# Kernel tuning notes

Hardware: AMD Instinct MI355X
Metric: run time of the kernel (lower is better)

Reference implementation:

```python
import jax, jax.numpy as jnp
import numpy as np

N, D_IN, D, K = 8192, 1024, 256, 30
SCALE = D ** (-0.5)


def setup_inputs() -> dict:
    key = jax.random.key(0)
    ks = jax.random.split(key, 10)
    p = lambda k, sh: (jax.random.normal(k, sh, dtype=jnp.float32) * 0.02)
    return {
        'x_path': jax.random.normal(ks[0], (N, D_IN), dtype=jnp.float32),
        'W_fc1': p(ks[1], (D_IN, D)), 'b_fc1': jnp.zeros((D,), jnp.float32),
        'W_fc2': p(ks[2], (D, D)),   'b_fc2': jnp.zeros((D,), jnp.float32),
        'W_head': p(ks[3], (D, D)),  'b_head': jnp.zeros((D,), jnp.float32),
        'W_tail': p(ks[4], (D, D)),  'b_tail': jnp.zeros((D,), jnp.float32),
        'W_lin1': p(ks[5], (D, D)),  'b_lin1': jnp.zeros((D,), jnp.float32),
        'W_lin2': p(ks[6], (D, D)),  'b_lin2': jnp.zeros((D,), jnp.float32),
        'W_att1': p(ks[7], (D, D // 2)), 'b_att1': jnp.zeros((D // 2,), jnp.float32),
        'W_att2': p(ks[8], (D // 2, 1)), 'b_att2': jnp.zeros((1,), jnp.float32),
    }


def reference(x_path, W_fc1, b_fc1, W_fc2, b_fc2, W_head, b_head, W_tail, b_tail,
              W_lin1, b_lin1, W_lin2, b_lin2, W_att1, b_att1, W_att2, b_att2):
    # pathology_fc (eval mode, dropout = identity): 1024 -> 256 -> 256
    h = jax.nn.relu(x_path @ W_fc1 + b_fc1)
    h = jax.nn.relu(h @ W_fc2 + b_fc2)                      # [N, D]

    e_h = h @ W_head + b_head                               # [N, D]
    e_t = h @ W_tail + b_tail                               # [N, D]

    # pairwise scores + topk neighbor selection
    attn_logit = (e_h * SCALE) @ e_t.T                      # [N, N]
    topk_w, topk_i = jax.lax.top_k(attn_logit, K)           # [N, K]
    topk_prob = jax.nn.softmax(topk_w, axis=-1)             # [N, K]

    Nb_h = e_t[topk_i]                                      # gather neighbors [N, K, D]

    # gated message construction
    eh_r = topk_prob[..., None] * Nb_h + (1.0 - topk_prob)[..., None] * e_h[:, None, :]
    gate = jnp.tanh(e_h[:, None, :] + eh_r)                 # [N, K, D]

    # torch.einsum('ijkl,ijkm->ijk', Nb_h, gate): l and m summed independently
    ka_weight = Nb_h.sum(-1) * gate.sum(-1)                 # [N, K]
    ka_prob = jax.nn.softmax(ka_weight, axis=-1)            # [N, K]
    e_Nh = jnp.einsum('nk,nkd->nd', ka_prob, Nb_h)          # [N, D]

    sum_emb = jax.nn.relu((e_h + e_Nh) @ W_lin1 + b_lin1)
    bi_emb = jax.nn.relu((e_h * e_Nh) @ W_lin2 + b_lin2)
    e = sum_emb + bi_emb                                    # [N, D]

    # GlobalAttention readout
    att = jax.nn.leaky_relu(e @ W_att1 + b_att1, 0.01) @ W_att2 + b_att2   # [N, 1]
    a = jax.nn.softmax(att, axis=0)                         # softmax over nodes
    e_g = (a * e).sum(0)                                    # [D]
    return e, e_g
```

## Files before the change

### kernel.cpp

```cpp
#include <hip/hip_runtime.h>
#include <math.h>

#define NN   8192
#define DIN  1024
#define DD   256
#define TOPK 30
#define KP   40
#define CAP  88
#define NINF -3e38f

typedef short s8v  __attribute__((ext_vector_type(8)));
typedef float f16v __attribute__((ext_vector_type(16)));

__device__ __forceinline__ float wred_sum(float v) {
  v += __shfl_down(v, 32); v += __shfl_down(v, 16); v += __shfl_down(v, 8);
  v += __shfl_down(v, 4);  v += __shfl_down(v, 2);  v += __shfl_down(v, 1);
  return v;
}
__device__ __forceinline__ float wred_max(float v) {
  v = fmaxf(v, __shfl_down(v, 32)); v = fmaxf(v, __shfl_down(v, 16));
  v = fmaxf(v, __shfl_down(v, 8));  v = fmaxf(v, __shfl_down(v, 4));
  v = fmaxf(v, __shfl_down(v, 2));  v = fmaxf(v, __shfl_down(v, 1));
  return v;
}
__device__ __forceinline__ float tanh_fast(float x) {
  return 1.f - 2.f / (__expf(2.f * x) + 1.f);
}
__device__ __forceinline__ unsigned short f2bf(float x) {
  union { float f; unsigned int u; } v; v.f = x;
  unsigned int r = v.u + 0x7FFF + ((v.u >> 16) & 1);
  return (unsigned short)(r >> 16);
}
__device__ __forceinline__ bool pair_gt(float v, int i, float pv, int pi) {
  return (v > pv) || (v == pv && i < pi);
}
__device__ __forceinline__ unsigned key_pack(float f, int col) {
  unsigned b = __float_as_uint(f);
  unsigned u = ((int)b < 0) ? ~b : (b | 0x80000000u);
  return (u & 0xFFFFE000u) | (unsigned)col;
}

template<int ACT, int AOP, int ACCUM>
__global__ __launch_bounds__(128, 4)
void gemm_k(const float* __restrict__ A, const float* __restrict__ A2,
            const float* __restrict__ B, const float* __restrict__ bias,
            float* __restrict__ C, int K, int NB)
{
  __shared__ float sA[32 * 36];
  __shared__ float sB[32 * 68];
  const int t  = threadIdx.x;
  const int rb = blockIdx.x * 32;
  const int cb = blockIdx.y * 64;
  const int tr = t >> 4;
  const int tc = t & 15;

  float acc[4][4];
#pragma unroll
  for (int u = 0; u < 4; ++u)
#pragma unroll
    for (int j = 0; j < 4; ++j) acc[u][j] = 0.f;

  const int sr  = t >> 2;
  const int sk2 = (t & 3) * 4;

  for (int kt = 0; kt < K; kt += 32) {
    __syncthreads();
    {
      const float* Ap = A + (size_t)(rb + sr) * K + kt;
      float4 va = *(const float4*)(Ap + sk2);
      float4 vb = *(const float4*)(Ap + sk2 + 16);
      if (AOP) {
        const float* A2p = A2 + (size_t)(rb + sr) * K + kt;
        const float4 wa = *(const float4*)(A2p + sk2);
        const float4 wb = *(const float4*)(A2p + sk2 + 16);
        if (AOP == 1) {
          va.x += wa.x; va.y += wa.y; va.z += wa.z; va.w += wa.w;
          vb.x += wb.x; vb.y += wb.y; vb.z += wb.z; vb.w += wb.w;
        } else {
          va.x *= wa.x; va.y *= wa.y; va.z *= wa.z; va.w *= wa.w;
          vb.x *= wb.x; vb.y *= wb.y; vb.z *= wb.z; vb.w *= wb.w;
        }
      }
      sA[(sk2 + 0) * 36 + sr] = va.x; sA[(sk2 + 1) * 36 + sr] = va.y;
      sA[(sk2 + 2) * 36 + sr] = va.z; sA[(sk2 + 3) * 36 + sr] = va.w;
      sA[(sk2 + 16) * 36 + sr] = vb.x; sA[(sk2 + 17) * 36 + sr] = vb.y;
      sA[(sk2 + 18) * 36 + sr] = vb.z; sA[(sk2 + 19) * 36 + sr] = vb.w;
    }
    {
#pragma unroll
      for (int i = 0; i < 4; ++i) {
        const int f4 = t + 128 * i;
        const int k  = f4 >> 4;
        const int c4 = (f4 & 15) << 2;
        *(float4*)&sB[k * 68 + c4] = *(const float4*)&B[(size_t)(kt + k) * NB + cb + c4];
      }
    }
    __syncthreads();
#pragma unroll 8
    for (int k = 0; k < 32; ++k) {
      const float4 bv = *(const float4*)&sB[k * 68 + 4 * tc];
      const float4 av = *(const float4*)&sA[k * 36 + 4 * tr];
      const float a[4] = {av.x, av.y, av.z, av.w};
      const float b[4] = {bv.x, bv.y, bv.z, bv.w};
#pragma unroll
      for (int u = 0; u < 4; ++u)
#pragma unroll
        for (int j = 0; j < 4; ++j) acc[u][j] = fmaf(a[u], b[j], acc[u][j]);
    }
  }

  const float4 bz = *(const float4*)&bias[cb + 4 * tc];
  const float bb[4] = {bz.x, bz.y, bz.z, bz.w};
#pragma unroll
  for (int u = 0; u < 4; ++u) {
    const int row = rb + 4 * tr + u;
    float o[4];
#pragma unroll
    for (int j = 0; j < 4; ++j) {
      o[j] = acc[u][j] + bb[j];
      if (ACT) o[j] = fmaxf(o[j], 0.f);
    }
    float* Cp = &C[(size_t)row * NB + cb + 4 * tc];
    if (ACCUM) {
      const float4 old = *(const float4*)Cp;
      o[0] += old.x; o[1] += old.y; o[2] += old.z; o[3] += old.w;
    }
    float4 ov; ov.x = o[0]; ov.y = o[1]; ov.z = o[2]; ov.w = o[3];
    *(float4*)Cp = ov;
  }
}

__global__ __launch_bounds__(256)
void pack_frag_k(const float* __restrict__ src, unsigned short* __restrict__ dst)
{
  const int c = blockIdx.x * 256 + threadIdx.x;
  const int l = c & 63;
  const int W = (c >> 6) & 15;
  const int T = c >> 10;
  const int col = T * 32 + (l & 31);
  const int k0  = W * 16 + ((l >> 5) << 3);
  const float4 a = *(const float4*)&src[(size_t)col * DD + k0];
  const float4 b = *(const float4*)&src[(size_t)col * DD + k0 + 4];
  uint4 o;
  o.x = (unsigned)f2bf(a.x) | ((unsigned)f2bf(a.y) << 16);
  o.y = (unsigned)f2bf(a.z) | ((unsigned)f2bf(a.w) << 16);
  o.z = (unsigned)f2bf(b.x) | ((unsigned)f2bf(b.y) << 16);
  o.w = (unsigned)f2bf(b.z) | ((unsigned)f2bf(b.w) << 16);
  *(uint4*)&dst[(size_t)c * 8] = o;
}

__global__ __launch_bounds__(256)
void rowsum_k(const float* __restrict__ et, float* __restrict__ rs)
{
  const int t = threadIdx.x, lane = t & 63, w = t >> 6;
  const int n = blockIdx.x * 4 + w;
  const float4 v = *(const float4*)&et[(size_t)n * DD + lane * 4];
  float s = v.x + v.y + v.z + v.w;
  s = wred_sum(s);
  if (lane == 0) rs[n] = s;
}

__global__ __launch_bounds__(512, 4)
void score_cand_k(const unsigned short* __restrict__ ehF,
                  const unsigned short* __restrict__ etF,
                  unsigned* __restrict__ gCand)
{
  __shared__ unsigned sBuf[32 * CAP];
  __shared__ unsigned sK[32][KP];
  __shared__ unsigned sThrK[32];
  __shared__ int      sCnt[32];

  const int t = threadIdx.x, lane = t & 63, w = t >> 6;
  const int g  = blockIdx.x;
  const int sy = blockIdx.y;
  const int tile0 = sy * 128;
  const s8v* eh8 = (const s8v*)ehF;
  const s8v* et8 = (const s8v*)etF;

  s8v af[16];
#pragma unroll
  for (int W = 0; W < 16; ++W)
    af[W] = eh8[((size_t)g * 16 + W) * 64 + lane];

  for (int idx = t; idx < 32 * KP; idx += 512) ((unsigned*)sK)[idx] = 0u;
  if (t < 32) { sThrK[t] = 0u; sCnt[t] = 0; }
  __syncthreads();

  const int rq = 4 * (lane >> 5);
  const int colLane = lane & 31;

  int tb = 0;
  for (int rnd = 0; rnd < 7; ++rnd) {
    const int ntile = (rnd == 0) ? 2 : (2 << (rnd - 1));
    for (int p = w; p < ntile; p += 8) {
      const int T = tile0 + tb + p;
      const s8v* bp = et8 + (size_t)T * 1024 + lane;
      f16v c;
#pragma unroll
      for (int i = 0; i < 16; ++i) c[i] = 0.f;
      {
        s8v b[8];
#pragma unroll
        for (int q = 0; q < 8; ++q) b[q] = bp[q * 64];
#pragma unroll
        for (int q = 0; q < 8; ++q)
          c = __builtin_amdgcn_mfma_f32_32x32x16_bf16(af[q], b[q], c, 0, 0, 0);
#pragma unroll
        for (int q = 0; q < 8; ++q) b[q] = bp[(8 + q) * 64];
#pragma unroll
        for (int q = 0; q < 8; ++q)
          c = __builtin_amdgcn_mfma_f32_32x32x16_bf16(af[8 + q], b[q], c, 0, 0, 0);
      }
      const int col = T * 32 + colLane;
#pragma unroll
      for (int r = 0; r < 16; ++r) {
        const int row = (r & 3) + 8 * (r >> 2) + rq;
        const unsigned key = key_pack(c[r], col);
        if (key > sThrK[row]) {
          const int ix = atomicAdd(&sCnt[row], 1);
          if (ix < CAP) sBuf[row * CAP + ix] = key;
        }
      }
    }
    __syncthreads();

#pragma unroll 1
    for (int rp = 0; rp < 2; ++rp) {
      const int ra = 4 * w + 2 * rp;
      const int rc = ra + 1;
      const int cA = min(sCnt[ra], CAP);
      const int cB = min(sCnt[rc], CAP);
      unsigned a0 = (lane < KP) ? sK[ra][lane]
                                : ((lane - KP) < cA ? sBuf[ra * CAP + (lane - KP)] : 0u);
      unsigned a1 = ((24 + lane) < cA) ? sBuf[ra * CAP + 24 + lane] : 0u;
      unsigned b0 = (lane < KP) ? sK[rc][lane]
                                : ((lane - KP) < cB ? sBuf[rc * CAP + (lane - KP)] : 0u);
      unsigned b1 = ((24 + lane) < cB) ? sBuf[rc * CAP + 24 + lane] : 0u;
#pragma unroll
      for (int k = 2; k <= 128; k <<= 1) {
#pragma unroll
        for (int j = k >> 1; j >= 1; j >>= 1) {
          if (j == 64) {
            unsigned mx = max(a0, a1), mn = min(a0, a1); a0 = mx; a1 = mn;
            mx = max(b0, b1); mn = min(b0, b1); b0 = mx; b1 = mn;
          } else {
            const unsigned pa0 = (unsigned)__shfl_xor((int)a0, j);
            const unsigned pa1 = (unsigned)__shfl_xor((int)a1, j);
            const unsigned pb0 = (unsigned)__shfl_xor((int)b0, j);
            const unsigned pb1 = (unsigned)__shfl_xor((int)b1, j);
            const bool km0 = (((lane & k) == 0)        == ((lane & j) == 0));
            const bool km1 = ((((64 + lane) & k) == 0) == ((lane & j) == 0));
            a0 = km0 ? max(a0, pa0) : min(a0, pa0);
            a1 = km1 ? max(a1, pa1) : min(a1, pa1);
            b0 = km0 ? max(b0, pb0) : min(b0, pb0);
            b1 = km1 ? max(b1, pb1) : min(b1, pb1);
          }
        }
      }
      if (rnd < 6) {
        if (lane < KP) { sK[ra][lane] = a0; sK[rc][lane] = b0; }
        if (lane == KP - 1) { sThrK[ra] = a0; sThrK[rc] = b0; }
        if (lane == 0) { sCnt[ra] = 0; sCnt[rc] = 0; }
      } else {
        if (lane < KP) {
          gCand[(((size_t)g * 2 + sy) * 32 + ra) * KP + lane] = a0;
          gCand[(((size_t)g * 2 + sy) * 32 + rc) * KP + lane] = b0;
        }
      }
    }
    __syncthreads();
    tb += ntile;
  }
}

__global__ __launch_bounds__(512, 2)
void cand_merge_k(const unsigned* __restrict__ gCand,
                  const float* __restrict__ e_h, const float* __restrict__ e_t,
                  float* __restrict__ topv_g, int* __restrict__ topi_g)
{
  __shared__ float    sEh[32 * 256];
  __shared__ unsigned sK40[32][KP];
  __shared__ float    sRes[32][KP];
  const int t = threadIdx.x, lane = t & 63, w = t >> 6;
  const int g = blockIdx.x, rb = g * 32;

  for (int i = t; i < 2048; i += 512)
    ((float4*)sEh)[i] = ((const float4*)(e_h + (size_t)rb * 256))[i];

#pragma unroll 1
  for (int rr = 0; rr < 4; ++rr) {
    const int r = 4 * w + rr;
    unsigned v0, v1;
    {
      const int m = lane;
      const int s = m / 40, q = m - s * 40;
      v0 = gCand[(((size_t)g * 2 + s) * 32 + r) * KP + q];
    }
    {
      const int m = 64 + lane;
      if (m < 80) {
        const int q = m - 40;
        v1 = gCand[(((size_t)g * 2 + 1) * 32 + r) * KP + q];
      } else v1 = 0u;
    }
#pragma unroll
    for (int k = 2; k <= 128; k <<= 1) {
#pragma unroll
      for (int j = k >> 1; j >= 1; j >>= 1) {
        if (j == 64) {
          const unsigned mx = max(v0, v1), mn = min(v0, v1);
          v0 = mx; v1 = mn;
        } else {
          const unsigned p0 = (unsigned)__shfl_xor((int)v0, j);
          const unsigned p1 = (unsigned)__shfl_xor((int)v1, j);
          const bool km0 = (((lane & k) == 0)        == ((lane & j) == 0));
          const bool km1 = ((((64 + lane) & k) == 0) == ((lane & j) == 0));
          v0 = km0 ? max(v0, p0) : min(v0, p0);
          v1 = km1 ? max(v1, p1) : min(v1, p1);
        }
      }
    }
    if (lane < KP) sK40[r][lane] = v0;
  }
  __syncthreads();

  for (int i = t; i < 32 * KP; i += 512) {
    const int r = i / KP, q = i - r * KP;
    const int c = (int)(sK40[r][q] & 0x1FFFu);
    const float* et = &e_t[(size_t)c * 256];
    const float* eh = &sEh[r * 256];
    float acc = 0.f;
#pragma unroll 8
    for (int d = 0; d < 64; ++d) {
      const float4 a = *(const float4*)&eh[d * 4];
      const float4 b = *(const float4*)&et[d * 4];
      acc = fmaf(a.x, b.x, acc); acc = fmaf(a.y, b.y, acc);
      acc = fmaf(a.z, b.z, acc); acc = fmaf(a.w, b.w, acc);
    }
    sRes[r][q] = acc * 0.0625f;
  }
  __syncthreads();

#pragma unroll 1
  for (int rr = 0; rr < 4; ++rr) {
    const int r = 4 * w + rr;
    float v; int c;
    if (lane < KP) { v = sRes[r][lane]; c = (int)(sK40[r][lane] & 0x1FFFu); }
    else           { v = NINF;          c = 0x40000000 + lane; }
#pragma unroll
    for (int k = 2; k <= 64; k <<= 1) {
#pragma unroll
      for (int j = k >> 1; j >= 1; j >>= 1) {
        const float pv = __shfl_xor(v, j);
        const int   pc = __shfl_xor(c, j);
        const bool km = (((lane & k) == 0) == ((lane & j) == 0));
        const bool gt = pair_gt(v, c, pv, pc);
        const bool keep = (km == gt);
        v = keep ? v : pv; c = keep ? c : pc;
      }
    }
    if (lane < TOPK) {
      topv_g[(size_t)(rb + r) * TOPK + lane] = v;
      topi_g[(size_t)(rb + r) * TOPK + lane] = c;
    }
  }
}

__global__ __launch_bounds__(256)
void message_k(const float* __restrict__ e_h, const float* __restrict__ e_t,
               const float* __restrict__ rs, const float* __restrict__ tv_g,
               const int* __restrict__ ti_g, float* __restrict__ e_Nh)
{
  __shared__ float sP[TOPK];
  __shared__ int   sI[TOPK];
  __shared__ float sW[TOPK];
  __shared__ float wpart[TOPK][4];
  const int n = blockIdx.x;
  const int t = threadIdx.x, lane = t & 63, w = t >> 6;

  if (w == 0) {
    const float v = (lane < TOPK) ? tv_g[(size_t)n * TOPK + lane] : NINF;
    float m = wred_max(v); m = __shfl(m, 0);
    const float p = (lane < TOPK) ? __expf(v - m) : 0.f;
    float s = wred_sum(p); s = __shfl(s, 0);
    if (lane < TOPK) { sP[lane] = p / s; sI[lane] = ti_g[(size_t)n * TOPK + lane]; }
  }
  __syncthreads();

  const float eh = e_h[(size_t)n * DD + t];
  float nbv[TOPK];
#pragma unroll
  for (int k = 0; k < TOPK; ++k) {
    const int   j = sI[k];
    const float p = sP[k];
    const float nb = e_t[(size_t)j * DD + t];
    nbv[k] = nb;
    float g = tanh_fast((2.f - p) * eh + p * nb);
    g = wred_sum(g);
    if (lane == 0) wpart[k][w] = g;
  }
  __syncthreads();

  if (w == 0) {
    float kw = NINF;
    if (lane < TOPK) {
      const float gs = wpart[lane][0] + wpart[lane][1] + wpart[lane][2] + wpart[lane][3];
      kw = rs[sI[lane]] * gs;
    }
    float m = wred_max(kw); m = __shfl(m, 0);
    const float p = (lane < TOPK) ? __expf(kw - m) : 0.f;
    float s = wred_sum(p); s = __shfl(s, 0);
    if (lane < TOPK) sW[lane] = p / s;
  }
  __syncthreads();

  float o = 0.f;
#pragma unroll
  for (int k = 0; k < TOPK; ++k) o = fmaf(sW[k], nbv[k], o);
  e_Nh[(size_t)n * DD + t] = o;
}

__global__ __launch_bounds__(256)
void att_k(const float* __restrict__ e, const float* __restrict__ W1,
           const float* __restrict__ b1, const float* __restrict__ W2,
           const float* __restrict__ b2, float* __restrict__ att)
{
  const int t = threadIdx.x;
  const int q = t >> 7;
  const int m = t & 127;
  const int lane = t & 63, w = t >> 6;
  const int n0 = blockIdx.x * 8 + q * 4;
  float acc[4] = {0.f, 0.f, 0.f, 0.f};
  for (int d = 0; d < DD; ++d) {
    const float wv = W1[d * 128 + m];
#pragma unroll
    for (int rr = 0; rr < 4; ++rr)
      acc[rr] = fmaf(e[(size_t)(n0 + rr) * DD + d], wv, acc[rr]);
  }
  const float b1m = b1[m], w2m = W2[m];
  __shared__ float part[4][4];
#pragma unroll
  for (int rr = 0; rr < 4; ++rr) {
    float v = acc[rr] + b1m;
    v = (v > 0.f) ? v : 0.01f * v;
    v *= w2m;
    v = wred_sum(v);
    if (lane == 0) part[w][rr] = v;
  }
  __syncthreads();
  if (t < 8) {
    const int qq = t >> 2, rr = t & 3;
    att[blockIdx.x * 8 + qq * 4 + rr] = part[qq * 2][rr] + part[qq * 2 + 1][rr] + b2[0];
  }
}

__global__ __launch_bounds__(1024)
void smax_prep_k(const float* __restrict__ att, float* __restrict__ stats,
                 float* __restrict__ eg)
{
  __shared__ float red[16];
  __shared__ float mg;
  const int t = threadIdx.x, lane = t & 63, w = t >> 6;
  float m = NINF;
#pragma unroll
  for (int i = 0; i < 8; ++i) m = fmaxf(m, att[t + 1024 * i]);
  m = wred_max(m);
  if (lane == 0) red[w] = m;
  __syncthreads();
  if (t == 0) {
    float mm = red[0];
    for (int i = 1; i < 16; ++i) mm = fmaxf(mm, red[i]);
    mg = mm;
  }
  __syncthreads();
  const float mm = mg;
  float s = 0.f;
#pragma unroll
  for (int i = 0; i < 8; ++i) s += __expf(att[t + 1024 * i] - mm);
  s = wred_sum(s);
  __syncthreads();
  if (lane == 0) red[w] = s;
  __syncthreads();
  if (t == 0) {
    float ss = 0.f;
    for (int i = 0; i < 16; ++i) ss += red[i];
    stats[0] = mm; stats[1] = ss;
  }
  if (t < DD) eg[t] = 0.f;
}

__global__ __launch_bounds__(256)
void eg_k(const float* __restrict__ att, const float* __restrict__ stats,
          const float* __restrict__ e, float* __restrict__ eg)
{
  const int t = threadIdx.x;
  const float m = stats[0], inv = 1.f / stats[1];
  float acc = 0.f;
  const int n0 = blockIdx.x * 128;
  for (int r = 0; r < 128; ++r) {
    const int n = n0 + r;
    acc = fmaf(__expf(att[n] - m), e[(size_t)n * DD + t], acc);
  }
  atomicAdd(&eg[t], acc * inv);
}

extern "C" void kernel_launch(void* const* d_in, const int* in_sizes, int n_in,
                              void* d_out, int out_size, void* d_ws, size_t ws_size,
                              hipStream_t stream)
{
  const float* x      = (const float*)d_in[0];
  const float* W_fc1  = (const float*)d_in[1];
  const float* b_fc1  = (const float*)d_in[2];
  const float* W_fc2  = (const float*)d_in[3];
  const float* b_fc2  = (const float*)d_in[4];
  const float* W_head = (const float*)d_in[5];
  const float* b_head = (const float*)d_in[6];
  const float* W_tail = (const float*)d_in[7];
  const float* b_tail = (const float*)d_in[8];
  const float* W_lin1 = (const float*)d_in[9];
  const float* b_lin1 = (const float*)d_in[10];
  const float* W_lin2 = (const float*)d_in[11];
  const float* b_lin2 = (const float*)d_in[12];
  const float* W_att1 = (const float*)d_in[13];
  const float* b_att1 = (const float*)d_in[14];
  const float* W_att2 = (const float*)d_in[15];
  const float* b_att2 = (const float*)d_in[16];

  float* out_e  = (float*)d_out;
  float* out_eg = out_e + (size_t)NN * DD;

  float* ws = (float*)d_ws;
  const size_t F = (size_t)NN * DD;
  float* e_h   = ws;
  float* e_t   = ws + F;
  float* e_Nh  = ws + 2 * F;
  float* bufA  = ws + 3 * F;
  float* bufB  = ws + 4 * F;
  float* rs    = ws + 5 * F;
  float* att   = rs + NN;
  float* stats = att + NN;
  float* topv  = stats + 16;
  int*   topi  = (int*)(topv + (size_t)NN * TOPK);

  unsigned short* ehF = (unsigned short*)bufA;
  unsigned short* etF = ehF + F;
  unsigned* gCand = (unsigned*)bufB;

  const dim3 blk(256);
  const dim3 gblk(128);
  const dim3 gemmGrid(NN / 32, DD / 64);

  gemm_k<1,0,0><<<gemmGrid, gblk, 0, stream>>>(x,    nullptr, W_fc1, b_fc1, bufA, DIN, DD);
  gemm_k<1,0,0><<<gemmGrid, gblk, 0, stream>>>(bufA, nullptr, W_fc2, b_fc2, bufB, DD,  DD);
  gemm_k<0,0,0><<<gemmGrid, gblk, 0, stream>>>(bufB, nullptr, W_head, b_head, e_h, DD, DD);
  gemm_k<0,0,0><<<gemmGrid, gblk, 0, stream>>>(bufB, nullptr, W_tail, b_tail, e_t, DD, DD);

  pack_frag_k<<<dim3(NN * DD / 8 / 256), blk, 0, stream>>>(e_h, ehF);
  pack_frag_k<<<dim3(NN * DD / 8 / 256), blk, 0, stream>>>(e_t, etF);
  rowsum_k<<<dim3(NN / 4), blk, 0, stream>>>(e_t, rs);

  score_cand_k<<<dim3(NN / 32, 2), dim3(512), 0, stream>>>(ehF, etF, gCand);
  cand_merge_k<<<dim3(NN / 32), dim3(512), 0, stream>>>(gCand, e_h, e_t, topv, topi);

  message_k<<<dim3(NN), blk, 0, stream>>>(e_h, e_t, rs, topv, topi, e_Nh);

  gemm_k<1,1,0><<<gemmGrid, gblk, 0, stream>>>(e_h, e_Nh, W_lin1, b_lin1, out_e, DD, DD);
  gemm_k<1,2,1><<<gemmGrid, gblk, 0, stream>>>(e_h, e_Nh, W_lin2, b_lin2, out_e, DD, DD);

  att_k<<<dim3(NN / 8), blk, 0, stream>>>(out_e, W_att1, b_att1, W_att2, b_att2, att);
  smax_prep_k<<<dim3(1), dim3(1024), 0, stream>>>(att, stats, out_eg);
  eg_k<<<dim3(64), blk, 0, stream>>>(att, stats, out_e, out_eg);
}
```

Measured before the change: 666.1 us.

## Retile fp32 GEMM, batch top-k candidate appends, split MFMA chains, halve merge block rows

The fp32 GEMM now uses 64-thread blocks, each thread computing an 8x4 output tile instead of 4x4, to raise register-level reuse. The score kernel keeps thresholds in registers per round, splits the MFMA chain into two independent accumulators, and replaces per-lane shared atomics with one wave-aggregated atomicAdd per half-wave using ballot and popcount. The candidate merge kernel handles 16 rows per block over a 2D grid, doubling the number of blocks. Risks: fewer waves per GEMM block can hurt latency hiding, and the register-cached thresholds are stale within a round, which may admit extra candidates.

```diff
diff --git a/kernel.cpp b/kernel.cpp
--- a/kernel.cpp
+++ b/kernel.cpp
@@ -41,7 +41,7 @@
 }
 
 template<int ACT, int AOP, int ACCUM>
-__global__ __launch_bounds__(128, 4)
+__global__ __launch_bounds__(64, 4)
 void gemm_k(const float* __restrict__ A, const float* __restrict__ A2,
             const float* __restrict__ B, const float* __restrict__ bias,
             float* __restrict__ C, int K, int NB)
@@ -51,59 +51,49 @@
   const int t  = threadIdx.x;
   const int rb = blockIdx.x * 32;
   const int cb = blockIdx.y * 64;
-  const int tr = t >> 4;
-  const int tc = t & 15;
-
-  float acc[4][4];
-#pragma unroll
-  for (int u = 0; u < 4; ++u)
+  const int tc  = t & 15;
+  const int trg = t >> 4;
+
+  float acc[8][4];
+#pragma unroll
+  for (int u = 0; u < 8; ++u)
 #pragma unroll
     for (int j = 0; j < 4; ++j) acc[u][j] = 0.f;
-
-  const int sr  = t >> 2;
-  const int sk2 = (t & 3) * 4;
 
   for (int kt = 0; kt < K; kt += 32) {
     __syncthreads();
-    {
-      const float* Ap = A + (size_t)(rb + sr) * K + kt;
-      float4 va = *(const float4*)(Ap + sk2);
-      float4 vb = *(const float4*)(Ap + sk2 + 16);
+#pragma unroll
+    for (int i = 0; i < 4; ++i) {
+      const int f   = t + 64 * i;
+      const int row = f >> 3;
+      const int kq  = (f & 7) << 2;
+      const float* Ap = A + (size_t)(rb + row) * K + kt + kq;
+      float4 va = *(const float4*)Ap;
       if (AOP) {
-        const float* A2p = A2 + (size_t)(rb + sr) * K + kt;
-        const float4 wa = *(const float4*)(A2p + sk2);
-        const float4 wb = *(const float4*)(A2p + sk2 + 16);
-        if (AOP == 1) {
-          va.x += wa.x; va.y += wa.y; va.z += wa.z; va.w += wa.w;
-          vb.x += wb.x; vb.y += wb.y; vb.z += wb.z; vb.w += wb.w;
-        } else {
-          va.x *= wa.x; va.y *= wa.y; va.z *= wa.z; va.w *= wa.w;
-          vb.x *= wb.x; vb.y *= wb.y; vb.z *= wb.z; vb.w *= wb.w;
-        }
-      }
-      sA[(sk2 + 0) * 36 + sr] = va.x; sA[(sk2 + 1) * 36 + sr] = va.y;
-      sA[(sk2 + 2) * 36 + sr] = va.z; sA[(sk2 + 3) * 36 + sr] = va.w;
-      sA[(sk2 + 16) * 36 + sr] = vb.x; sA[(sk2 + 17) * 36 + sr] = vb.y;
-      sA[(sk2 + 18) * 36 + sr] = vb.z; sA[(sk2 + 19) * 36 + sr] = vb.w;
-    }
-    {
-#pragma unroll
-      for (int i = 0; i < 4; ++i) {
-        const int f4 = t + 128 * i;
-        const int k  = f4 >> 4;
-        const int c4 = (f4 & 15) << 2;
-        *(float4*)&sB[k * 68 + c4] = *(const float4*)&B[(size_t)(kt + k) * NB + cb + c4];
-      }
+        const float4 wa = *(const float4*)(A2 + (size_t)(rb + row) * K + kt + kq);
+        if (AOP == 1) { va.x += wa.x; va.y += wa.y; va.z += wa.z; va.w += wa.w; }
+        else          { va.x *= wa.x; va.y *= wa.y; va.z *= wa.z; va.w *= wa.w; }
+      }
+      sA[(kq + 0) * 36 + row] = va.x; sA[(kq + 1) * 36 + row] = va.y;
+      sA[(kq + 2) * 36 + row] = va.z; sA[(kq + 3) * 36 + row] = va.w;
+    }
+#pragma unroll
+    for (int i = 0; i < 8; ++i) {
+      const int f  = t + 64 * i;
+      const int k  = f >> 4;
+      const int c4 = (f & 15) << 2;
+      *(float4*)&sB[k * 68 + c4] = *(const float4*)&B[(size_t)(kt + k) * NB + cb + c4];
     }
     __syncthreads();
-#pragma unroll 8
+#pragma unroll 4
     for (int k = 0; k < 32; ++k) {
       const float4 bv = *(const float4*)&sB[k * 68 + 4 * tc];
-      const float4 av = *(const float4*)&sA[k * 36 + 4 * tr];
-      const float a[4] = {av.x, av.y, av.z, av.w};
+      const float4 a0 = *(const float4*)&sA[k * 36 + 8 * trg];
+      const float4 a1 = *(const float4*)&sA[k * 36 + 8 * trg + 4];
+      const float a[8] = {a0.x, a0.y, a0.z, a0.w, a1.x, a1.y, a1.z, a1.w};
       const float b[4] = {bv.x, bv.y, bv.z, bv.w};
 #pragma unroll
-      for (int u = 0; u < 4; ++u)
+      for (int u = 0; u < 8; ++u)
 #pragma unroll
         for (int j = 0; j < 4; ++j) acc[u][j] = fmaf(a[u], b[j], acc[u][j]);
     }
@@ -112,8 +102,8 @@
   const float4 bz = *(const float4*)&bias[cb + 4 * tc];
   const float bb[4] = {bz.x, bz.y, bz.z, bz.w};
 #pragma unroll
-  for (int u = 0; u < 4; ++u) {
-    const int row = rb + 4 * tr + u;
+  for (int u = 0; u < 8; ++u) {
+    const int row = rb + 8 * trg + u;
     float o[4];
 #pragma unroll
     for (int j = 0; j < 4; ++j) {
@@ -188,36 +178,45 @@
 
   const int rq = 4 * (lane >> 5);
   const int colLane = lane & 31;
+  const int half = lane >> 5;
+  const int leader = half << 5;
+  const unsigned lm = (1u << (lane & 31)) - 1;
 
   int tb = 0;
   for (int rnd = 0; rnd < 7; ++rnd) {
     const int ntile = (rnd == 0) ? 2 : (2 << (rnd - 1));
+    float dummy; (void)dummy;
+    unsigned thrv[16];
+#pragma unroll
+    for (int r = 0; r < 16; ++r) thrv[r] = sThrK[(r & 3) + 8 * (r >> 2) + rq];
+
     for (int p = w; p < ntile; p += 8) {
       const int T = tile0 + tb + p;
       const s8v* bp = et8 + (size_t)T * 1024 + lane;
-      f16v c;
-#pragma unroll
-      for (int i = 0; i < 16; ++i) c[i] = 0.f;
-      {
-        s8v b[8];
-#pragma unroll
-        for (int q = 0; q < 8; ++q) b[q] = bp[q * 64];
-#pragma unroll
-        for (int q = 0; q < 8; ++q)
-          c = __builtin_amdgcn_mfma_f32_32x32x16_bf16(af[q], b[q], c, 0, 0, 0);
-#pragma unroll
-        for (int q = 0; q < 8; ++q) b[q] = bp[(8 + q) * 64];
-#pragma unroll
-        for (int q = 0; q < 8; ++q)
-          c = __builtin_amdgcn_mfma_f32_32x32x16_bf16(af[8 + q], b[q], c, 0, 0, 0);
+      s8v b[16];
+#pragma unroll
+      for (int q = 0; q < 16; ++q) b[q] = bp[q * 64];
+      f16v c0, c1;
+#pragma unroll
+      for (int i = 0; i < 16; ++i) { c0[i] = 0.f; c1[i] = 0.f; }
+#pragma unroll
+      for (int q = 0; q < 8; ++q) {
+        c0 = __builtin_amdgcn_mfma_f32_32x32x16_bf16(af[q],     b[q],     c0, 0, 0, 0);
+        c1 = __builtin_amdgcn_mfma_f32_32x32x16_bf16(af[8 + q], b[8 + q], c1, 0, 0, 0);
       }
       const int col = T * 32 + colLane;
 #pragma unroll
       for (int r = 0; r < 16; ++r) {
         const int row = (r & 3) + 8 * (r >> 2) + rq;
-        const unsigned key = key_pack(c[r], col);
-        if (key > sThrK[row]) {
-          const int ix = atomicAdd(&sCnt[row], 1);
+        const unsigned key = key_pack(c0[r] + c1[r], col);
+        const bool pass = key > thrv[r];
+        const unsigned long long mask = __ballot(pass);
+        const unsigned hm = (unsigned)(mask >> leader);
+        int base = 0;
+        if ((lane & 31) == 0) base = atomicAdd(&sCnt[row], __popc(hm));
+        base = __shfl(base, leader);
+        if (pass) {
+          const int ix = base + __popc(hm & lm);
           if (ix < CAP) sBuf[row * CAP + ix] = key;
         }
       }
@@ -278,18 +277,20 @@
                   const float* __restrict__ e_h, const float* __restrict__ e_t,
                   float* __restrict__ topv_g, int* __restrict__ topi_g)
 {
-  __shared__ float    sEh[32 * 256];
-  __shared__ unsigned sK40[32][KP];
-  __shared__ float    sRes[32][KP];
+  __shared__ float    sEh[16 * 256];
+  __shared__ unsigned sK40[16][KP];
+  __shared__ float    sRes[16][KP];
   const int t = threadIdx.x, lane = t & 63, w = t >> 6;
   const int g = blockIdx.x, rb = g * 32;
-
-  for (int i = t; i < 2048; i += 512)
-    ((float4*)sEh)[i] = ((const float4*)(e_h + (size_t)rb * 256))[i];
+  const int r0 = blockIdx.y * 16;
+
+  for (int i = t; i < 1024; i += 512)
+    ((float4*)sEh)[i] = ((const float4*)(e_h + (size_t)(rb + r0) * 256))[i];
 
 #pragma unroll 1
-  for (int rr = 0; rr < 4; ++rr) {
-    const int r = 4 * w + rr;
+  for (int rp = 0; rp < 2; ++rp) {
+    const int lr = 2 * w + rp;
+    const int r  = r0 + lr;
     unsigned v0, v1;
     {
       const int m = lane;
@@ -320,15 +321,15 @@
         }
       }
     }
-    if (lane < KP) sK40[r][lane] = v0;
-  }
-  __syncthreads();
-
-  for (int i = t; i < 32 * KP; i += 512) {
-    const int r = i / KP, q = i - r * KP;
-    const int c = (int)(sK40[r][q] & 0x1FFFu);
+    if (lane < KP) sK40[lr][lane] = v0;
+  }
+  __syncthreads();
+
+  for (int i = t; i < 16 * KP; i += 512) {
+    const int lr = i / KP, q = i - lr * KP;
+    const int c = (int)(sK40[lr][q] & 0x1FFFu);
     const float* et = &e_t[(size_t)c * 256];
-    const float* eh = &sEh[r * 256];
+    const float* eh = &sEh[lr * 256];
     float acc = 0.f;
 #pragma unroll 8
     for (int d = 0; d < 64; ++d) {
@@ -337,16 +338,16 @@
       acc = fmaf(a.x, b.x, acc); acc = fmaf(a.y, b.y, acc);
       acc = fmaf(a.z, b.z, acc); acc = fmaf(a.w, b.w, acc);
     }
-    sRes[r][q] = acc * 0.0625f;
+    sRes[lr][q] = acc * 0.0625f;
   }
   __syncthreads();
 
 #pragma unroll 1
-  for (int rr = 0; rr < 4; ++rr) {
-    const int r = 4 * w + rr;
+  for (int rp = 0; rp < 2; ++rp) {
+    const int lr = 2 * w + rp;
     float v; int c;
-    if (lane < KP) { v = sRes[r][lane]; c = (int)(sK40[r][lane] & 0x1FFFu); }
-    else           { v = NINF;          c = 0x40000000 + lane; }
+    if (lane < KP) { v = sRes[lr][lane]; c = (int)(sK40[lr][lane] & 0x1FFFu); }
+    else           { v = NINF;           c = 0x40000000 + lane; }
 #pragma unroll
     for (int k = 2; k <= 64; k <<= 1) {
 #pragma unroll
@@ -360,8 +361,8 @@
       }
     }
     if (lane < TOPK) {
-      topv_g[(size_t)(rb + r) * TOPK + lane] = v;
-      topi_g[(size_t)(rb + r) * TOPK + lane] = c;
+      topv_g[(size_t)(rb + r0 + lr) * TOPK + lane] = v;
+      topi_g[(size_t)(rb + r0 + lr) * TOPK + lane] = c;
     }
   }
 }
@@ -547,7 +548,7 @@
   unsigned* gCand = (unsigned*)bufB;
 
   const dim3 blk(256);
-  const dim3 gblk(128);
+  const dim3 gblk(64);
   const dim3 gemmGrid(NN / 32, DD / 64);
 
   gemm_k<1,0,0><<<gemmGrid, gblk, 0, stream>>>(x,    nullptr, W_fc1, b_fc1, bufA, DIN, DD);
@@ -560,7 +561,7 @@
   rowsum_k<<<dim3(NN / 4), blk, 0, stream>>>(e_t, rs);
 
   score_cand_k<<<dim3(NN / 32, 2), dim3(512), 0, stream>>>(ehF, etF, gCand);
-  cand_merge_k<<<dim3(NN / 32), dim3(512), 0, stream>>>(gCand, e_h, e_t, topv, topi);
+  cand_merge_k<<<dim3(NN / 32, 2), dim3(512), 0, stream>>>(gCand, e_h, e_t, topv, topi);
 
   message_k<<<dim3(NN), blk, 0, stream>>>(e_h, e_t, rs, topv, topi, e_Nh);
 
```

Result: slower. 738.0 us (+10.8%).
